# Kernel tuning notes

Hardware: AMD Instinct MI355X
Metric: run time of the kernel (lower is better)

The kernel has to match this reference:

```python
import jax, jax.numpy as jnp
import numpy as np

CANVAS = 512
SCORE_THR = 0.02
NMS_THR = 0.45
LVTOP = 1000      # cfg['lvtop'] for mm source
IMTOP = 200       # cfg['imtop']
NMS_PRE = 2000    # fixed pre-NMS candidate cap (static shape for jit)
NUM_CLASSES = 80
STRIDES = [8, 16, 32, 64, 128, 256, 512]
AR3 = [False, True, True, True, True, False, False]


def _make_priors():
    # get_scales(512): smallest=0.04, rmin=0.1, rmax=0.9, n=7
    smallest, rmin, rmax, n = 0.04, 0.1, 0.9, 7
    step = (rmax - rmin) / (n - 2)
    scales = [smallest] + [rmin + i * step for i in range(n)]
    sz = np.round(np.array(scales) * CANVAS).astype(np.int64)
    pr, lvlen = [], []
    for i, s in enumerate(STRIDES):
        fs = CANVAS // s
        ratios = [1.0, 2.0, 0.5] + ([3.0, 1.0 / 3.0] if AR3[i] else [])
        wh = [(sz[i] * np.sqrt(r), sz[i] / np.sqrt(r)) for r in ratios]
        extra = np.sqrt(float(sz[i]) * float(sz[i + 1]))  # sqrt(sz[i+1]/sz[i])*sz[i]
        wh.insert(1, (extra, extra))
        wh = np.array(wh, np.float32)            # [na, 2]
        xs = (np.arange(fs, dtype=np.float32) + 0.5) * s
        cx, cy = np.meshgrid(xs, xs)             # rows index y
        ctr = np.stack([cx, cy], -1)[:, :, None, :]  # [fs, fs, 1, 2]
        na = wh.shape[0]
        p = np.concatenate([np.broadcast_to(ctr, (fs, fs, na, 2)),
                            np.broadcast_to(wh, (fs, fs, na, 2))], -1).reshape(-1, 4)
        pr.append(p)
        lvlen.append(p.shape[0])
    return np.concatenate(pr).astype(np.float32), lvlen

PRIORS_NP, LVLEN = _make_priors()   # total 24564, lvlen=[16384,6144,1536,384,96,16,4]


def setup_inputs() -> dict:
    key = jax.random.key(0)
    k1, k2 = jax.random.split(key)
    A = PRIORS_NP.shape[0]
    cls_logits = jax.random.normal(k1, (4, A, NUM_CLASSES + 1), dtype=jnp.float32)
    reg = jax.random.normal(k2, (4, A, 4), dtype=jnp.float32)
    priors = jnp.asarray(PRIORS_NP)
    return {"cls_logits": cls_logits, "reg": reg, "priors": priors}


def _pairwise_iou(b):  # b: [K,4] xyxy
    area = (b[:, 2] - b[:, 0]) * (b[:, 3] - b[:, 1])
    lt = jnp.maximum(b[:, None, :2], b[None, :, :2])
    rb = jnp.minimum(b[:, None, 2:], b[None, :, 2:])
    wh = jnp.clip(rb - lt, 0.0)
    inter = wh[..., 0] * wh[..., 1]
    return inter / jnp.maximum(area[:, None] + area[None, :] - inter, 1e-6)


def _nms_keep(b):  # boxes sorted by descending score, class-offset applied
    m = _pairwise_iou(b) * jnp.triu(jnp.ones((NMS_PRE, NMS_PRE), b.dtype), 1)
    def body(sup, i):
        sup = sup | ((~sup[i]) & (m[i] > NMS_THR))
        return sup, None
    sup, _ = jax.lax.scan(body, jnp.zeros((NMS_PRE,), bool), jnp.arange(NMS_PRE))
    return ~sup


def reference(cls_logits, reg, priors):
    N = cls_logits.shape[0]
    C = NUM_CLASSES
    # softmax, background class is LAST (bckg_class_first=False for mm source)
    scr = jax.nn.softmax(cls_logits, axis=-1)[..., :-1]
    scr = jnp.where(scr > SCORE_THR, scr, 0.0)  # score threshold (fidx filter)
    # per-level top-k over flattened (anchor, class) pairs  [post.top_per_level]
    vals_l, anch_l, cls_l = [], [], []
    start = 0
    for lv in LVLEN:
        f = scr[:, start:start + lv, :].reshape(N, lv * C)
        k = min(LVTOP, lv * C)
        v, idx = jax.lax.top_k(f, k)
        vals_l.append(v)
        anch_l.append(start + idx // C)
        cls_l.append(idx % C)
        start += lv
    vals = jnp.concatenate(vals_l, 1)
    anch = jnp.concatenate(anch_l, 1)
    cls = jnp.concatenate(cls_l, 1)
    # fixed-size pre-NMS cap (static shapes under jit)
    v2, sel = jax.lax.top_k(vals, NMS_PRE)
    anch = jnp.take_along_axis(anch, sel, 1)
    cls = jnp.take_along_axis(cls, sel, 1)
    # decode boxes  [post.decode_boxes, mults=(0.1, 0.2), clamp=True]
    p = priors[anch]                                 # [N,K,4] cxcywh
    r = jnp.take_along_axis(reg, anch[..., None], 1)  # [N,K,4]
    cx = p[..., 0] + r[..., 0] * 0.1 * p[..., 2]
    cy = p[..., 1] + r[..., 1] * 0.1 * p[..., 3]
    w = p[..., 2] * jnp.exp(r[..., 2] * 0.2)
    h = p[..., 3] * jnp.exp(r[..., 3] * 0.2)
    boxes = jnp.stack([cx - w / 2, cy - h / 2, cx + w / 2, cy + h / 2], -1)
    boxes = jnp.clip(boxes, 0.0, float(CANVAS))
    # class-aware NMS via class offsets
    nb = boxes + cls.astype(boxes.dtype)[..., None] * (2.0 * CANVAS)
    keep = jax.vmap(_nms_keep)(nb)                   # [N,K] bool
    fs = jnp.where(keep & (v2 > 0), v2, 0.0)
    fv, fi = jax.lax.top_k(fs, IMTOP)                # imtop
    fb = jnp.take_along_axis(boxes, fi[..., None], 1)
    fc = jnp.take_along_axis(cls, fi, 1)
    fb = jnp.where(fv[..., None] > 0, fb, 0.0)
    return fb, fv, fc
```

## Files before the change

### kernel.cpp

```cpp
#include <hip/hip_runtime.h>
#include <hip/hip_bf16.h>
#include <math.h>

typedef unsigned long long u64;
typedef unsigned int u32;

#define A_TOTAL 24564
#define NCLS 80
#define NIMG 4
#define NPRE 2000
#define NLV 7
#define HBUCKETS 1024
#define BEXP_BASE 0x3CA3
#define TOTAL_G (NIMG * A_TOTAL)
#define FA 64
#define FT 256
#define NBLK_F ((TOTAL_G + FA - 1) / FA)
#define POOL_CAP_MAX 4096
#define CAPSEL 4608

__device__ __constant__ int c_klv[NLV] = {1000,1000,1000,1000,1000,1000,320};

#define WS_HIST      0
#define WS_MCOUNT    114688
#define WS_BCOUNT    114800
#define WS_ZERO_END  114912
#define WS_PCOUNT    114912
#define WS_MAIN      121280
#define WS_BND       350656
#define WS_BOXES     1268160
#define WS_CLS       1396160
#define WS_SCORE     1428160
#define WS_MASK      1460160
#define WS_POOL      3508160

#define NZERO_W (WS_ZERO_END / 4)

__device__ inline u64 shfl_u64(u64 v, int src) {
  int lo = __shfl((int)(u32)(v & 0xFFFFFFFFULL), src);
  int hi = __shfl((int)(u32)(v >> 32), src);
  return ((u64)(u32)hi << 32) | (u32)lo;
}

__device__ inline int score_bucket(u32 bits) {
  int b = (int)(bits >> 16) - BEXP_BASE;
  return b < 0 ? 0 : (b > HBUCKETS - 1 ? HBUCKETS - 1 : b);
}

__device__ inline int level_of(int a) {
  return (a < 16384) ? 0 : (a < 22528) ? 1 : (a < 24064) ? 2 :
         (a < 24448) ? 3 : (a < 24544) ? 4 : (a < 24560) ? 5 : 6;
}

__global__ __launch_bounds__(256) void k_zero(u32* __restrict__ p) {
  int i = blockIdx.x * 256 + threadIdx.x;
  if (i < NZERO_W) p[i] = 0;
}

__device__ inline void score20(const float* __restrict__ logits, int g, int q,
                               float (&e)[20], float& rt) {
  const float* row = logits + (size_t)g * 81;
  float x[20];
#pragma unroll
  for (int i = 0; i < 20; ++i) x[i] = row[q * 20 + i];
  float x80 = (q == 3) ? row[80] : 0.f;
  float mloc = x[0];
#pragma unroll
  for (int i = 1; i < 20; ++i) mloc = fmaxf(mloc, x[i]);
  if (q == 3) mloc = fmaxf(mloc, x80);
  float m = fmaxf(mloc, __shfl_xor(mloc, 1));
  m = fmaxf(m, __shfl_xor(m, 2));
  float tq = 0.f;
#pragma unroll
  for (int i = 0; i < 20; ++i) { e[i] = expf(x[i] - m); tq += e[i]; }
  if (q == 3) tq += expf(x80 - m);
  float t = tq + __shfl_xor(tq, 1);
  t = t + __shfl_xor(t, 2);
  rt = 1.0f / t;
}

__device__ inline void wave_find_cut(const u32* __restrict__ h, int k, int lane,
                                     int& cx, int& cy) {
  u32 s = 0;
#pragma unroll
  for (int i = 0; i < 16; ++i) s += h[lane * 16 + i];
  u32 S = s;
#pragma unroll
  for (int o = 1; o < 64; o <<= 1) {
    u32 t = (u32)__shfl_down((int)S, o);
    if (lane + o < 64) S += t;
  }
  u32 total = (u32)__shfl((int)S, 0);
  if (total <= (u32)k) { cx = -1; cy = 0; return; }
  u64 bm = __ballot(S >= (u32)k);
  int L0 = 63 - (int)__clzll((long long)bm);
  u32 Sup = (u32)__shfl_down((int)S, 1);
  if (lane == 63) Sup = 0;
  int rcx = 0, rcy = 0;
  if (lane == L0) {
    u32 cum = Sup;
    for (int i = 15; i >= 0; --i) {
      u32 c = h[lane * 16 + i];
      if (cum + c >= (u32)k) { rcx = lane * 16 + i; rcy = k - (int)cum; break; }
      cum += c;
    }
  }
  cx = __shfl(rcx, L0);
  cy = __shfl(rcy, L0);
}

__global__ __launch_bounds__(FT) void k_fused(const float* __restrict__ logits,
                                              u32* __restrict__ histG,
                                              u64* __restrict__ pool,
                                              u32* __restrict__ pcount, int cap) {
  __shared__ u32 sh[HBUCKETS];
  __shared__ int nm;
  int tid = threadIdx.x, bx = blockIdx.x;
  for (int b = tid; b < HBUCKETS; b += FT) sh[b] = 0;
  if (tid == 0) nm = 0;
  int la = tid >> 2, q = tid & 3;
  int g = bx * FA + la;
  bool valid = g < TOTAL_G;
  int g0 = bx * FA;
  int seg0 = (g0 / A_TOTAL) * NLV + level_of(g0 % A_TOTAL);
  int seg = seg0, a = 0;
  float e[20];
  float rt = 0.f;
  if (valid) {
    int img = g / A_TOTAL;
    a = g - img * A_TOTAL;
    seg = img * NLV + level_of(a);
    score20(logits, g, q, e, rt);
  }
  int uniform = __syncthreads_and((int)(!valid || seg == seg0));
  if (valid) {
    u32* hdst = uniform ? sh : (histG + (size_t)seg * HBUCKETS);
    int c0 = q * 20;
    u32 wmask = 0;
#pragma unroll
    for (int i = 0; i < 20; ++i) {
      float s = e[i] * rt;
      if (s > 0.02f) wmask |= (1u << i);
    }
    int cnt = __popc(wmask);
    int basep = 0;
    if (cnt) basep = atomicAdd(&nm, cnt);
    while (wmask) {
      int i = __ffs(wmask) - 1;
      wmask &= wmask - 1;
      float s = e[i] * rt;
      u32 bits = __float_as_uint(s);
      atomicAdd(&hdst[score_bucket(bits)], 1u);
      if (basep < cap)
        pool[(size_t)bx * cap + basep] =
            ((u64)bits << 32) | (u64)(0xFFFFFFFFu - (u32)(a * NCLS + c0 + i));
      ++basep;
    }
  }
  __syncthreads();
  if (uniform) {
    u32* hseg = histG + (size_t)seg0 * HBUCKETS;
    for (int b = tid; b < HBUCKETS; b += FT) {
      u32 v = sh[b];
      if (v) atomicAdd(&hseg[b], v);
    }
  }
  if (tid == 0) pcount[bx] = (u32)nm;
}

__global__ __launch_bounds__(FT) void k_filter(const float* __restrict__ logits,
                                               const u64* __restrict__ pool,
                                               const u32* __restrict__ pcount,
                                               const u32* __restrict__ histG, int cap,
                                               u64* __restrict__ mainG, u32* __restrict__ mcount,
                                               u64* __restrict__ bndG, u32* __restrict__ bcount) {
  __shared__ int lcx4[4];
  __shared__ u64 mk[1024]; __shared__ unsigned char msg_[1024];
  __shared__ u64 bkl[256]; __shared__ unsigned char bsg[256];
  __shared__ int nm, nb, cm[4], cb[4], basem[4], baseb[4], wm[4], wb[4];
  int tid = threadIdx.x, bx = blockIdx.x;
  if (tid < 4) { cm[tid] = 0; cb[tid] = 0; wm[tid] = 0; wb[tid] = 0; }
  if (tid == 0) { nm = 0; nb = 0; }
  int g0 = bx * FA;
  int img0 = g0 / A_TOTAL;
  int alo = g0 - img0 * A_TOTAL;
  int gN = g0 + FA - 1; if (gN > TOTAL_G - 1) gN = TOTAL_G - 1;
  int seg_lo = img0 * NLV + level_of(alo);
  int seg_hi = (gN / A_TOTAL) * NLV + level_of(gN % A_TOTAL);
  int nseg = seg_hi - seg_lo + 1;
  int wid = tid >> 6, lane = tid & 63;
  if (wid < nseg) {
    int cx, cy;
    wave_find_cut(histG + (size_t)(seg_lo + wid) * HBUCKETS,
                  c_klv[(seg_lo + wid) % NLV], lane, cx, cy);
    if (lane == 0) lcx4[wid] = cx;
  }
  __syncthreads();
  int n = (int)pcount[bx];
  if (n <= cap) {
    for (int t = tid; t < n; t += FT) {
      u64 key = pool[(size_t)bx * cap + t];
      u32 bits = (u32)(key >> 32);
      u32 flat = 0xFFFFFFFFu - (u32)(key & 0xFFFFFFFFULL);
      int a = (int)(flat / NCLS);
      int img = (a >= alo) ? img0 : img0 + 1;
      int seg = img * NLV + level_of(a);
      int si = seg - seg_lo;
      int ctx = lcx4[si];
      int bk = score_bucket(bits);
      if (ctx < 0 || bk > ctx) {
        int p = atomicAdd(&nm, 1);
        if (p < 1024) { mk[p] = key; msg_[p] = (unsigned char)si; atomicAdd(&cm[si], 1); }
        else { u32 pg = atomicAdd(&mcount[seg], 1u); if (pg < 1024) mainG[(size_t)seg * 1024 + pg] = key; }
      } else if (bk == ctx) {
        int p = atomicAdd(&nb, 1);
        if (p < 256) { bkl[p] = key; bsg[p] = (unsigned char)si; atomicAdd(&cb[si], 1); }
        else { u32 pg = atomicAdd(&bcount[seg], 1u); if (pg < 4096) bndG[(size_t)seg * 4096 + pg] = key; }
      }
    }
  } else {
    int la = tid >> 2, q = tid & 3;
    int g = g0 + la;
    if (g < TOTAL_G) {
      int img = g / A_TOTAL;
      int a = g - img * A_TOTAL;
      int seg = img * NLV + level_of(a);
      int si = seg - seg_lo;
      int ctx = lcx4[si];
      float e[20];
      float rt;
      score20(logits, g, q, e, rt);
      int c0 = q * 20;
      for (int i = 0; i < 20; ++i) {
        float s = e[i] * rt;
        if (s > 0.02f) {
          u32 bits = __float_as_uint(s);
          int bk = score_bucket(bits);
          u64 key = ((u64)bits << 32) | (u64)(0xFFFFFFFFu - (u32)(a * NCLS + c0 + i));
          if (ctx < 0 || bk > ctx) {
            int p = atomicAdd(&nm, 1);
            if (p < 1024) { mk[p] = key; msg_[p] = (unsigned char)si; atomicAdd(&cm[si], 1); }
            else { u32 pg = atomicAdd(&mcount[seg], 1u); if (pg < 1024) mainG[(size_t)seg * 1024 + pg] = key; }
          } else if (bk == ctx) {
            int p = atomicAdd(&nb, 1);
            if (p < 256) { bkl[p] = key; bsg[p] = (unsigned char)si; atomicAdd(&cb[si], 1); }
            else { u32 pg = atomicAdd(&bcount[seg], 1u); if (pg < 4096) bndG[(size_t)seg * 4096 + pg] = key; }
          }
        }
      }
    }
  }
  __syncthreads();
  if (tid < nseg) {
    if (cm[tid] > 0) basem[tid] = (int)atomicAdd(&mcount[seg_lo + tid], (u32)cm[tid]);
    if (cb[tid] > 0) baseb[tid] = (int)atomicAdd(&bcount[seg_lo + tid], (u32)cb[tid]);
  }
  __syncthreads();
  int tm = nm < 1024 ? nm : 1024;
  for (int idx = tid; idx < tm; idx += FT) {
    int si = msg_[idx];
    int slot = atomicAdd(&wm[si], 1);
    int d = basem[si] + slot;
    if (d < 1024) mainG[(size_t)(seg_lo + si) * 1024 + d] = mk[idx];
  }
  int tb = nb < 256 ? nb : 256;
  for (int idx = tid; idx < tb; idx += FT) {
    int si = bsg[idx];
    int slot = atomicAdd(&wb[si], 1);
    int d = baseb[si] + slot;
    if (d < 4096) bndG[(size_t)(seg_lo + si) * 4096 + d] = bkl[idx];
  }
}

__device__ inline void bitonic_desc(u64* s, int n) {
  for (int k = 2; k <= n; k <<= 1)
    for (int j = k >> 1; j > 0; j >>= 1) {
      __syncthreads();
      for (int i = threadIdx.x; i < n; i += blockDim.x) {
        int l = i ^ j;
        if (l > i) {
          u64 a = s[i], b = s[l];
          if (((i & k) == 0) ? (a < b) : (a > b)) { s[i] = b; s[l] = a; }
        }
      }
    }
  __syncthreads();
}

__global__ __launch_bounds__(1024) void k_refine(const u32* __restrict__ histG,
                                                 const u64* __restrict__ bndG,
                                                 const u32* __restrict__ bcount,
                                                 u64* __restrict__ mainG, u32* __restrict__ mcount) {
  int seg = blockIdx.x;
  __shared__ int sh_cx, sh_cy;
  __shared__ u64 s[4096];
  int tid = threadIdx.x, lane = tid & 63;
  if (tid < 64) {
    int cx, cy;
    wave_find_cut(histG + (size_t)seg * HBUCKETS, c_klv[seg % NLV], lane, cx, cy);
    if (lane == 0) { sh_cx = cx; sh_cy = cy; }
  }
  __syncthreads();
  if (sh_cx < 0) return;
  int m = (int)bcount[seg]; if (m > 4096) m = 4096;
  int n = 64; while (n < m) n <<= 1;
  for (int t = tid; t < n; t += 1024)
    s[t] = (t < m) ? bndG[(size_t)seg * 4096 + t] : 0ULL;
  bitonic_desc(s, n);
  int kp = sh_cy; if (kp > m) kp = m;
  int base = (int)mcount[seg];
  for (int t = tid; t < kp; t += 1024) {
    int p = base + t;
    if (p < 1024) mainG[(size_t)seg * 1024 + p] = s[t];
  }
  __syncthreads();
  if (tid == 0) {
    int nb = base + kp;
    mcount[seg] = (u32)(nb > 1024 ? 1024 : nb);
  }
}

__global__ __launch_bounds__(1024) void k_gsel(const u32* __restrict__ histG,
                                               const u64* __restrict__ mainG,
                                               const u32* __restrict__ mcount,
                                               const float4* __restrict__ priors,
                                               const float4* __restrict__ reg,
                                               float4* __restrict__ boxesG,
                                               int* __restrict__ clsG,
                                               float* __restrict__ scoreG) {
  int img = blockIdx.x;
  int tid = threadIdx.x, wid = tid >> 6, lane = tid & 63;
  __shared__ u32 H[HBUCKETS];
  __shared__ u32 cntb[HBUCKETS];
  __shared__ u32 Sarr[HBUCKETS];
  __shared__ u32 cnt2[HBUCKETS];
  __shared__ u64 sel[CAPSEL];
  __shared__ int lcx[NLV], lcy[NLV];
  __shared__ int sh_gx, sh_gy, sh_cC, sh_cand, sh_sgx;
  if (tid == 0) { sh_cC = 0; sh_cand = 0; sh_sgx = -1; }
  if (wid < NLV) {
    int cx, cy;
    wave_find_cut(histG + (size_t)(img * NLV + wid) * HBUCKETS, c_klv[wid], lane, cx, cy);
    if (lane == 0) { lcx[wid] = cx; lcy[wid] = cy; }
  }
  __syncthreads();
  for (int b = tid; b < HBUCKETS; b += 1024) {
    u32 acc = 0;
#pragma unroll
    for (int l = 0; l < NLV; ++l) {
      u32 h = histG[(size_t)(img * NLV + l) * HBUCKETS + b];
      int cx = lcx[l];
      if (cx < 0 || b > cx) acc += h;
      else if (b == cx) acc += (u32)lcy[l];
    }
    H[b] = acc;
    cntb[b] = 0;
    cnt2[b] = 0;
  }
  __syncthreads();
  if (wid == 0) {
    int gx, gy;
    wave_find_cut(H, NPRE, lane, gx, gy);
    if (lane == 0) { sh_gx = gx; sh_gy = gy; }
  }
  __syncthreads();
  int gx = sh_gx, gy = sh_gy;
  int mcap[NLV];
#pragma unroll
  for (int l = 0; l < NLV; ++l) { int c = (int)mcount[img * NLV + l]; mcap[l] = c > 1024 ? 1024 : c; }
  for (int l = 0; l < NLV; ++l)
    for (int t = tid; t < mcap[l]; t += 1024) {
      u64 key = mainG[(size_t)(img * NLV + l) * 1024 + t];
      int b = score_bucket((u32)(key >> 32));
      if (gx < 0 || b > gx) atomicAdd(&cntb[b], 1u);
      else if (b == gx) atomicAdd(&sh_cC, 1);
    }
  __syncthreads();
  for (int b = tid; b < HBUCKETS; b += 1024) Sarr[b] = cntb[b];
  __syncthreads();
  {
    u32* A = Sarr; u32* B = H;
    for (int o = 1; o < HBUCKETS; o <<= 1) {
      for (int b = tid; b < HBUCKETS; b += 1024)
        B[b] = A[b] + ((b + o < HBUCKETS) ? A[b + o] : 0u);
      __syncthreads();
      u32* tmp = A; A = B; B = tmp;
    }
  }
  int cA = (int)Sarr[0];
  int cC = sh_cC;
  int cand = (gx >= 0) ? cC : 0;
  int sgx = -1;
  if (gx >= 0 && cA + cC > CAPSEL) {
    for (int b = tid; b < HBUCKETS; b += 1024) H[b] = 0;
    __syncthreads();
    for (int l = 0; l < NLV; ++l)
      for (int t = tid; t < mcap[l]; t += 1024) {
        u64 key = mainG[(size_t)(img * NLV + l) * 1024 + t];
        u32 bits = (u32)(key >> 32);
        if (score_bucket(bits) == gx) atomicAdd(&H[(bits >> 6) & 1023], 1u);
      }
    __syncthreads();
    if (wid == 0) {
      int a1, a2;
      wave_find_cut(H, gy, lane, a1, a2);
      if (lane == 0) sh_sgx = a1;
    }
    __syncthreads();
    sgx = sh_sgx;
    if (sgx >= 0) {
      for (int s2 = tid; s2 < HBUCKETS; s2 += 1024)
        if (s2 >= sgx) { u32 v = H[s2]; if (v) atomicAdd(&sh_cand, (int)v); }
      __syncthreads();
      cand = sh_cand;
    }
    if (cA + cand > CAPSEL) cand = CAPSEL - cA;
  }
  __syncthreads();
  for (int l = 0; l < NLV; ++l)
    for (int t = tid; t < mcap[l]; t += 1024) {
      u64 key = mainG[(size_t)(img * NLV + l) * 1024 + t];
      u32 bits = (u32)(key >> 32);
      int b = score_bucket(bits);
      bool inc = false; int segbase = 0, seglen = 0;
      if (gx < 0 || b > gx) {
        inc = true; segbase = (int)(Sarr[b] - cntb[b]); seglen = (int)cntb[b];
      } else if (b == gx) {
        inc = (sgx < 0) || ((int)((bits >> 6) & 1023) >= sgx);
        segbase = (int)Sarr[b]; seglen = cand;
      }
      if (inc) {
        int slot = (int)atomicAdd(&cnt2[b], 1u);
        if (slot < seglen) sel[segbase + slot] = key;
      }
    }
  __syncthreads();
  int total = cA + cand;
  u64 myk[5]; int myp[5];
#pragma unroll
  for (int it = 0; it < 5; ++it) {
    int t = tid + it * 1024;
    myp[it] = -1; myk[it] = 0;
    if (t < total) {
      u64 key = sel[t];
      u32 bits = (u32)(key >> 32);
      int b = score_bucket(bits);
      int segbase, seglen;
      if (gx >= 0 && b == gx) { segbase = (int)Sarr[b]; seglen = cand; }
      else { segbase = (int)(Sarr[b] - cntb[b]); seglen = (int)cntb[b]; }
      int r = 0;
      for (int u = 0; u < seglen; ++u) r += (sel[segbase + u] > key) ? 1 : 0;
      myk[it] = key; myp[it] = segbase + r;
    }
  }
  __syncthreads();
#pragma unroll
  for (int it = 0; it < 5; ++it) if (myp[it] >= 0) sel[myp[it]] = myk[it];
  __syncthreads();
  for (int t = tid; t < NPRE; t += 1024) {
    u64 key = (t < total) ? sel[t] : 0ULL;
    float4 bx = make_float4(0.f, 0.f, 0.f, 0.f);
    int c = -1;
    float sc = 0.f;
    if (key != 0ULL) {
      sc = __uint_as_float((u32)(key >> 32));
      u32 flat = 0xFFFFFFFFu - (u32)(key & 0xFFFFFFFFULL);
      int a = (int)(flat / NCLS);
      c = (int)(flat % NCLS);
      float4 p = priors[a];
      float4 r = reg[(size_t)img * A_TOTAL + a];
      float cx = p.x + (r.x * 0.1f) * p.z;
      float cy = p.y + (r.y * 0.1f) * p.w;
      float w = p.z * expf(r.z * 0.2f);
      float h = p.w * expf(r.w * 0.2f);
      bx.x = fminf(fmaxf(cx - w * 0.5f, 0.f), 512.f);
      bx.y = fminf(fmaxf(cy - h * 0.5f, 0.f), 512.f);
      bx.z = fminf(fmaxf(cx + w * 0.5f, 0.f), 512.f);
      bx.w = fminf(fmaxf(cy + h * 0.5f, 0.f), 512.f);
    }
    boxesG[(size_t)img * NPRE + t] = bx;
    clsG[(size_t)img * NPRE + t] = c;
    scoreG[(size_t)img * NPRE + t] = sc;
  }
}

__global__ __launch_bounds__(256) void k_mask(const float4* __restrict__ boxesG,
                                              const int* __restrict__ clsG,
                                              u64* __restrict__ maskG) {
  __shared__ float4 lb[NPRE];
  __shared__ int lc[NPRE];
  int img = blockIdx.x / 500;
  int rb = (blockIdx.x % 500) * 4;
  for (int t = threadIdx.x; t < NPRE; t += 256) {
    lb[t] = boxesG[(size_t)img * NPRE + t];
    lc[t] = clsG[(size_t)img * NPRE + t];
  }
  __syncthreads();
  int w = threadIdx.x >> 6, lane = threadIdx.x & 63;
  int i = rb + w;
  float4 bi = lb[i];
  int ci = lc[i];
  float ai = (bi.z - bi.x) * (bi.w - bi.y);
  u64* mrow = maskG + ((size_t)img * NPRE + i) * 32;
  for (int ch = 0; ch < 32; ++ch) {
    int j = ch * 64 + lane;
    bool pred = false;
    if (j < NPRE && j > i) {
      if (lc[j] == ci) {
        float4 bj = lb[j];
        float xx1 = fmaxf(bi.x, bj.x), yy1 = fmaxf(bi.y, bj.y);
        float xx2 = fminf(bi.z, bj.z), yy2 = fminf(bi.w, bj.w);
        float ww = fmaxf(xx2 - xx1, 0.f), hh = fmaxf(yy2 - yy1, 0.f);
        float inter = ww * hh;
        float aj = (bj.z - bj.x) * (bj.w - bj.y);
        float iou = inter / fmaxf(ai + aj - inter, 1e-6f);
        pred = iou > 0.45f;
      }
    }
    u64 word = __ballot(pred);
    if (lane == 0) mrow[ch] = word;
  }
}

__global__ __launch_bounds__(256) void k_scanfinal(const u64* __restrict__ maskG,
                                                   const float4* __restrict__ boxesG,
                                                   const int* __restrict__ clsG,
                                                   const float* __restrict__ scoreG,
                                                   float* __restrict__ out) {
  int img = blockIdx.x;
  int tid = threadIdx.x;
  __shared__ u64 sh_remv[32];
  __shared__ u32 keptList[216];
  __shared__ int sh_cnt, sh_done;
  __shared__ int kpref[257];
  __shared__ unsigned short S[NPRE];
  if (tid == 0) { sh_cnt = 0; sh_done = 0; }
  __syncthreads();
  if (tid < 64) {
    int lane = tid;
    int wl = lane & 31;
    const u64* M = maskG + (size_t)img * NPRE * 32;
    u64 remv = 0;
    u64 cur[16], nxt[16];
    int cnt = 0;
#pragma unroll
    for (int r = 0; r < 16; ++r) cur[r] = M[(size_t)r * 32 + wl];
    int t = 0;
    for (; t < 125; ++t) {
      if (t < 124) {
#pragma unroll
        for (int r = 0; r < 16; ++r) nxt[r] = M[(size_t)((t + 1) * 16 + r) * 32 + wl];
      }
#pragma unroll
      for (int r = 0; r < 16; ++r) {
        int i = t * 16 + r;
        u64 rm = shfl_u64(remv, i >> 6);
        if (!((rm >> (i & 63)) & 1ULL)) {
          remv |= cur[r];
          if (lane == 0 && cnt < 216) keptList[cnt] = (u32)i;
          ++cnt;
        }
      }
#pragma unroll
      for (int r = 0; r < 16; ++r) cur[r] = nxt[r];
      if (cnt >= 200) { ++t; break; }
    }
    if (lane == 0) sh_cnt = cnt < 216 ? cnt : 216;
    if (t >= 125) {
      if (lane == 0) sh_done = 1;
      if (lane < 32) sh_remv[lane] = remv;
    }
  }
  __syncthreads();
  int nK = sh_cnt;
  if (sh_done && nK < 200) {
    int base = tid * 8;
    bool sb[8];
    int scnt = 0;
#pragma unroll
    for (int e = 0; e < 8; ++e) {
      int i = base + e;
      bool sup = (i < NPRE) && ((sh_remv[i >> 6] >> (i & 63)) & 1ULL);
      sb[e] = sup;
      scnt += sup ? 1 : 0;
    }
    kpref[tid + 1] = scnt;
    if (tid == 0) kpref[0] = 0;
    __syncthreads();
    if (tid == 0) {
      int acc = 0;
      for (int t = 1; t <= 256; ++t) { acc += kpref[t]; kpref[t] = acc; }
    }
    __syncthreads();
    int sp = kpref[tid];
#pragma unroll
    for (int e = 0; e < 8; ++e) {
      int i = base + e;
      if (i < NPRE && sb[e]) S[sp++] = (unsigned short)i;
    }
    __syncthreads();
    if (tid < 200) {
      float fv = 0.f;
      float4 fb = make_float4(0.f, 0.f, 0.f, 0.f);
      int fc;
      if (tid < nK) {
        int idx = (int)keptList[tid];
        fv = scoreG[(size_t)img * NPRE + idx];
        fb = boxesG[(size_t)img * NPRE + idx];
        fc = clsG[(size_t)img * NPRE + idx];
      } else {
        int idx = S[tid - nK];
        fc = clsG[(size_t)img * NPRE + idx];
      }
      float* fbo = out + (size_t)img * 800 + tid * 4;
      fbo[0] = fb.x; fbo[1] = fb.y; fbo[2] = fb.z; fbo[3] = fb.w;
      out[3200 + (size_t)img * 200 + tid] = fv;
      out[4000 + (size_t)img * 200 + tid] = (float)fc;
    }
  } else {
    if (tid < 200) {
      int idx = (int)keptList[tid];
      float fv = scoreG[(size_t)img * NPRE + idx];
      float4 fb = boxesG[(size_t)img * NPRE + idx];
      int fc = clsG[(size_t)img * NPRE + idx];
      float* fbo = out + (size_t)img * 800 + tid * 4;
      fbo[0] = fb.x; fbo[1] = fb.y; fbo[2] = fb.z; fbo[3] = fb.w;
      out[3200 + (size_t)img * 200 + tid] = fv;
      out[4000 + (size_t)img * 200 + tid] = (float)fc;
    }
  }
}

extern "C" void kernel_launch(void* const* d_in, const int* in_sizes, int n_in,
                              void* d_out, int out_size, void* d_ws, size_t ws_size,
                              hipStream_t stream) {
  const float* logits = (const float*)d_in[0];
  const float4* reg = (const float4*)d_in[1];
  const float4* priors = (const float4*)d_in[2];
  char* ws = (char*)d_ws;
  u32* hist = (u32*)(ws + WS_HIST);
  u32* mcount = (u32*)(ws + WS_MCOUNT);
  u32* bcount = (u32*)(ws + WS_BCOUNT);
  u32* pcount = (u32*)(ws + WS_PCOUNT);
  u64* mainL = (u64*)(ws + WS_MAIN);
  u64* bndL = (u64*)(ws + WS_BND);
  float4* boxes = (float4*)(ws + WS_BOXES);
  int* cls = (int*)(ws + WS_CLS);
  float* score = (float*)(ws + WS_SCORE);
  u64* mask = (u64*)(ws + WS_MASK);
  u64* pool = (u64*)(ws + WS_POOL);

  size_t avail = ws_size > (size_t)WS_POOL ? ws_size - (size_t)WS_POOL : 0;
  int cap = (int)(avail / ((size_t)NBLK_F * 8));
  if (cap > POOL_CAP_MAX) cap = POOL_CAP_MAX;

  k_zero<<<(NZERO_W + 255) / 256, 256, 0, stream>>>((u32*)d_ws);
  k_fused<<<NBLK_F, FT, 0, stream>>>(logits, hist, pool, pcount, cap);
  k_filter<<<NBLK_F, FT, 0, stream>>>(logits, pool, pcount, hist, cap,
                                      mainL, mcount, bndL, bcount);
  k_refine<<<28, 1024, 0, stream>>>(hist, bndL, bcount, mainL, mcount);
  k_gsel<<<NIMG, 1024, 0, stream>>>(hist, mainL, mcount, priors, reg, boxes, cls, score);
  k_mask<<<NIMG * 500, 256, 0, stream>>>(boxes, cls, mask);
  k_scanfinal<<<NIMG, 256, 0, stream>>>(mask, boxes, cls, score, (float*)d_out);
}
```

Measured before the change: 113.5 us.

## Fuse IoU mask computation and greedy NMS scan into one per-image kernel

Replaces the separate mask kernel (2000 blocks writing a full 2000x2000 bitmask to global memory) and the scan kernel with one 1024-thread block per image. Wave 0 runs the greedy suppression scan over 16-row chunks while the other 15 waves compute the next chunk's IoU mask rows into a double-buffered shared-memory buffer. Mask computation also stops early once 200 boxes are kept. This removes the global mask traffic and a kernel launch, but leaves only 4 blocks on the GPU and adds a block-wide barrier per chunk.

Measured after the change: 211.7 us. 86.4% more time.

```diff
diff --git a/kernel.cpp b/kernel.cpp
--- a/kernel.cpp
+++ b/kernel.cpp
@@ -18,6 +18,7 @@
 #define NBLK_F ((TOTAL_G + FA - 1) / FA)
 #define POOL_CAP_MAX 4096
 #define CAPSEL 4608
+#define NMST 1024
 
 __device__ __constant__ int c_klv[NLV] = {1000,1000,1000,1000,1000,1000,320};
 
@@ -31,7 +32,6 @@
 #define WS_BOXES     1268160
 #define WS_CLS       1396160
 #define WS_SCORE     1428160
-#define WS_MASK      1460160
 #define WS_POOL      3508160
 
 #define NZERO_W (WS_ZERO_END / 4)
@@ -484,29 +484,36 @@
   }
 }
 
-__global__ __launch_bounds__(256) void k_mask(const float4* __restrict__ boxesG,
+__global__ __launch_bounds__(NMST) void k_nms(const float4* __restrict__ boxesG,
                                               const int* __restrict__ clsG,
-                                              u64* __restrict__ maskG) {
+                                              const float* __restrict__ scoreG,
+                                              float* __restrict__ out) {
+  int img = blockIdx.x;
+  int tid = threadIdx.x, wid = tid >> 6, lane = tid & 63;
   __shared__ float4 lb[NPRE];
-  __shared__ int lc[NPRE];
-  int img = blockIdx.x / 500;
-  int rb = (blockIdx.x % 500) * 4;
-  for (int t = threadIdx.x; t < NPRE; t += 256) {
+  __shared__ short lc2[NPRE];
+  __shared__ u64 mbuf[2][16][32];
+  __shared__ u64 sh_remv[32];
+  __shared__ u32 keptList[216];
+  __shared__ int sh_cnt, sh_done, sh_stop;
+  __shared__ int kpref[NMST + 1];
+  __shared__ unsigned short S[NPRE];
+  if (tid == 0) { sh_cnt = 0; sh_done = 0; sh_stop = 0; }
+  for (int t = tid; t < NPRE; t += NMST) {
     lb[t] = boxesG[(size_t)img * NPRE + t];
-    lc[t] = clsG[(size_t)img * NPRE + t];
-  }
-  __syncthreads();
-  int w = threadIdx.x >> 6, lane = threadIdx.x & 63;
-  int i = rb + w;
-  float4 bi = lb[i];
-  int ci = lc[i];
-  float ai = (bi.z - bi.x) * (bi.w - bi.y);
-  u64* mrow = maskG + ((size_t)img * NPRE + i) * 32;
-  for (int ch = 0; ch < 32; ++ch) {
-    int j = ch * 64 + lane;
-    bool pred = false;
-    if (j < NPRE && j > i) {
-      if (lc[j] == ci) {
+    lc2[t] = (short)clsG[(size_t)img * NPRE + t];
+  }
+  __syncthreads();
+
+  auto row_mask = [&](int t, int buf, int r) {
+    int i = t * 16 + r;
+    float4 bi = lb[i];
+    short ci = lc2[i];
+    float ai = (bi.z - bi.x) * (bi.w - bi.y);
+    for (int c = 0; c < 32; ++c) {
+      int j = c * 64 + lane;
+      bool pred = false;
+      if (j > i && lc2[j] == ci) {
         float4 bj = lb[j];
         float xx1 = fmaxf(bi.x, bj.x), yy1 = fmaxf(bi.y, bj.y);
         float xx2 = fminf(bi.z, bj.z), yy2 = fminf(bi.w, bj.w);
@@ -516,88 +523,63 @@
         float iou = inter / fmaxf(ai + aj - inter, 1e-6f);
         pred = iou > 0.45f;
       }
-    }
-    u64 word = __ballot(pred);
-    if (lane == 0) mrow[ch] = word;
-  }
-}
-
-__global__ __launch_bounds__(256) void k_scanfinal(const u64* __restrict__ maskG,
-                                                   const float4* __restrict__ boxesG,
-                                                   const int* __restrict__ clsG,
-                                                   const float* __restrict__ scoreG,
-                                                   float* __restrict__ out) {
-  int img = blockIdx.x;
-  int tid = threadIdx.x;
-  __shared__ u64 sh_remv[32];
-  __shared__ u32 keptList[216];
-  __shared__ int sh_cnt, sh_done;
-  __shared__ int kpref[257];
-  __shared__ unsigned short S[NPRE];
-  if (tid == 0) { sh_cnt = 0; sh_done = 0; }
-  __syncthreads();
-  if (tid < 64) {
-    int lane = tid;
-    int wl = lane & 31;
-    const u64* M = maskG + (size_t)img * NPRE * 32;
-    u64 remv = 0;
-    u64 cur[16], nxt[16];
-    int cnt = 0;
-#pragma unroll
-    for (int r = 0; r < 16; ++r) cur[r] = M[(size_t)r * 32 + wl];
-    int t = 0;
-    for (; t < 125; ++t) {
-      if (t < 124) {
-#pragma unroll
-        for (int r = 0; r < 16; ++r) nxt[r] = M[(size_t)((t + 1) * 16 + r) * 32 + wl];
-      }
-#pragma unroll
+      u64 word = __ballot(pred);
+      if (lane == 0) mbuf[buf][r][c] = word;
+    }
+  };
+
+  row_mask(0, 0, wid);
+  __syncthreads();
+
+  u64 remv = 0;
+  int cnt = 0;
+  int t = 0;
+  while (true) {
+    if (wid > 0 && t + 1 < 125) {
+      for (int r = wid - 1; r < 16; r += 15) row_mask(t + 1, (t + 1) & 1, r);
+    }
+    if (wid == 0) {
+      int wl = lane & 31;
       for (int r = 0; r < 16; ++r) {
         int i = t * 16 + r;
+        u64 cur = mbuf[t & 1][r][wl];
         u64 rm = shfl_u64(remv, i >> 6);
         if (!((rm >> (i & 63)) & 1ULL)) {
-          remv |= cur[r];
+          remv |= cur;
           if (lane == 0 && cnt < 216) keptList[cnt] = (u32)i;
           ++cnt;
         }
       }
-#pragma unroll
-      for (int r = 0; r < 16; ++r) cur[r] = nxt[r];
-      if (cnt >= 200) { ++t; break; }
-    }
-    if (lane == 0) sh_cnt = cnt < 216 ? cnt : 216;
-    if (t >= 125) {
-      if (lane == 0) sh_done = 1;
-      if (lane < 32) sh_remv[lane] = remv;
-    }
-  }
-  __syncthreads();
+      if (lane == 0 && (cnt >= 200 || t == 124)) {
+        sh_stop = 1;
+        sh_cnt = cnt < 216 ? cnt : 216;
+        if (cnt < 200 && t == 124) sh_done = 1;
+      }
+      if (t == 124 && lane < 32) sh_remv[lane] = remv;
+    }
+    __syncthreads();
+    if (sh_stop) break;
+    ++t;
+  }
+
   int nK = sh_cnt;
   if (sh_done && nK < 200) {
-    int base = tid * 8;
-    bool sb[8];
+    int base = tid * 2;
+    bool sb0 = false, sb1 = false;
     int scnt = 0;
-#pragma unroll
-    for (int e = 0; e < 8; ++e) {
-      int i = base + e;
-      bool sup = (i < NPRE) && ((sh_remv[i >> 6] >> (i & 63)) & 1ULL);
-      sb[e] = sup;
-      scnt += sup ? 1 : 0;
-    }
+    if (base < NPRE)     { sb0 = (sh_remv[base >> 6] >> (base & 63)) & 1ULL; scnt += sb0 ? 1 : 0; }
+    if (base + 1 < NPRE) { sb1 = (sh_remv[(base + 1) >> 6] >> ((base + 1) & 63)) & 1ULL; scnt += sb1 ? 1 : 0; }
     kpref[tid + 1] = scnt;
     if (tid == 0) kpref[0] = 0;
     __syncthreads();
     if (tid == 0) {
       int acc = 0;
-      for (int t = 1; t <= 256; ++t) { acc += kpref[t]; kpref[t] = acc; }
+      for (int i = 1; i <= NMST; ++i) { acc += kpref[i]; kpref[i] = acc; }
     }
     __syncthreads();
     int sp = kpref[tid];
-#pragma unroll
-    for (int e = 0; e < 8; ++e) {
-      int i = base + e;
-      if (i < NPRE && sb[e]) S[sp++] = (unsigned short)i;
-    }
+    if (base < NPRE && sb0) S[sp++] = (unsigned short)base;
+    if (base + 1 < NPRE && sb1) S[sp++] = (unsigned short)(base + 1);
     __syncthreads();
     if (tid < 200) {
       float fv = 0.f;
@@ -606,11 +588,11 @@
       if (tid < nK) {
         int idx = (int)keptList[tid];
         fv = scoreG[(size_t)img * NPRE + idx];
-        fb = boxesG[(size_t)img * NPRE + idx];
-        fc = clsG[(size_t)img * NPRE + idx];
+        fb = lb[idx];
+        fc = (int)lc2[idx];
       } else {
         int idx = S[tid - nK];
-        fc = clsG[(size_t)img * NPRE + idx];
+        fc = (int)lc2[idx];
       }
       float* fbo = out + (size_t)img * 800 + tid * 4;
       fbo[0] = fb.x; fbo[1] = fb.y; fbo[2] = fb.z; fbo[3] = fb.w;
@@ -621,8 +603,8 @@
     if (tid < 200) {
       int idx = (int)keptList[tid];
       float fv = scoreG[(size_t)img * NPRE + idx];
-      float4 fb = boxesG[(size_t)img * NPRE + idx];
-      int fc = clsG[(size_t)img * NPRE + idx];
+      float4 fb = lb[idx];
+      int fc = (int)lc2[idx];
       float* fbo = out + (size_t)img * 800 + tid * 4;
       fbo[0] = fb.x; fbo[1] = fb.y; fbo[2] = fb.z; fbo[3] = fb.w;
       out[3200 + (size_t)img * 200 + tid] = fv;
@@ -647,7 +629,6 @@
   float4* boxes = (float4*)(ws + WS_BOXES);
   int* cls = (int*)(ws + WS_CLS);
   float* score = (float*)(ws + WS_SCORE);
-  u64* mask = (u64*)(ws + WS_MASK);
   u64* pool = (u64*)(ws + WS_POOL);
 
   size_t avail = ws_size > (size_t)WS_POOL ? ws_size - (size_t)WS_POOL : 0;
@@ -660,6 +641,5 @@
                                       mainL, mcount, bndL, bcount);
   k_refine<<<28, 1024, 0, stream>>>(hist, bndL, bcount, mainL, mcount);
   k_gsel<<<NIMG, 1024, 0, stream>>>(hist, mainL, mcount, priors, reg, boxes, cls, score);
-  k_mask<<<NIMG * 500, 256, 0, stream>>>(boxes, cls, mask);
-  k_scanfinal<<<NIMG, 256, 0, stream>>>(mask, boxes, cls, score, (float*)d_out);
-}
+  k_nms<<<NIMG, NMST, 0, stream>>>(boxes, cls, score, (float*)d_out);
+}
```

## Compute NMS mask only for first 512 rows with on-demand fallback

Applied to the files above, without the earlier changes.

The IoU suppression mask kernel now computes only the first 512 candidate rows per image instead of all 2000, which cuts its grid size roughly fourfold. The scan kernel walks these precomputed rows; if fewer than 200 boxes are kept by then, it computes the remaining rows tile by tile inside the scan block, reading boxes from global memory. Class ids are also stored as shorts in shared memory. The fallback path is slow and serialized but only runs when early termination fails.

Measured after the change: 107.3 us, median of 2. -5.5%, faster.

```diff
diff --git a/kernel.cpp b/kernel.cpp
--- a/kernel.cpp
+++ b/kernel.cpp
@@ -18,6 +18,8 @@
 #define NBLK_F ((TOTAL_G + FA - 1) / FA)
 #define POOL_CAP_MAX 4096
 #define CAPSEL 4608
+#define MROWS 512
+#define FTILES (MROWS / 16)
 
 __device__ __constant__ int c_klv[NLV] = {1000,1000,1000,1000,1000,1000,320};
 
@@ -488,20 +490,20 @@
                                               const int* __restrict__ clsG,
                                               u64* __restrict__ maskG) {
   __shared__ float4 lb[NPRE];
-  __shared__ int lc[NPRE];
-  int img = blockIdx.x / 500;
-  int rb = (blockIdx.x % 500) * 4;
+  __shared__ short lc[NPRE];
+  int img = blockIdx.x / (MROWS / 4);
+  int rb = (blockIdx.x % (MROWS / 4)) * 4;
   for (int t = threadIdx.x; t < NPRE; t += 256) {
     lb[t] = boxesG[(size_t)img * NPRE + t];
-    lc[t] = clsG[(size_t)img * NPRE + t];
+    lc[t] = (short)clsG[(size_t)img * NPRE + t];
   }
   __syncthreads();
   int w = threadIdx.x >> 6, lane = threadIdx.x & 63;
   int i = rb + w;
   float4 bi = lb[i];
-  int ci = lc[i];
+  short ci = lc[i];
   float ai = (bi.z - bi.x) * (bi.w - bi.y);
-  u64* mrow = maskG + ((size_t)img * NPRE + i) * 32;
+  u64* mrow = maskG + ((size_t)img * MROWS + i) * 32;
   for (int ch = 0; ch < 32; ++ch) {
     int j = ch * 64 + lane;
     bool pred = false;
@@ -529,25 +531,25 @@
                                                    float* __restrict__ out) {
   int img = blockIdx.x;
   int tid = threadIdx.x;
+  int wid = tid >> 6, lane = tid & 63;
   __shared__ u64 sh_remv[32];
+  __shared__ u64 fbm[16][32];
   __shared__ u32 keptList[216];
-  __shared__ int sh_cnt, sh_done;
+  __shared__ int sh_cnt, sh_done, sh_fall, sh_stop;
   __shared__ int kpref[257];
   __shared__ unsigned short S[NPRE];
-  if (tid == 0) { sh_cnt = 0; sh_done = 0; }
-  __syncthreads();
+  if (tid == 0) { sh_cnt = 0; sh_done = 0; sh_fall = 0; sh_stop = 0; }
+  __syncthreads();
+  u64 remv = 0;
+  int cnt = 0;
   if (tid < 64) {
-    int lane = tid;
     int wl = lane & 31;
-    const u64* M = maskG + (size_t)img * NPRE * 32;
-    u64 remv = 0;
+    const u64* M = maskG + (size_t)img * MROWS * 32;
     u64 cur[16], nxt[16];
-    int cnt = 0;
 #pragma unroll
     for (int r = 0; r < 16; ++r) cur[r] = M[(size_t)r * 32 + wl];
-    int t = 0;
-    for (; t < 125; ++t) {
-      if (t < 124) {
+    for (int t = 0; t < FTILES; ++t) {
+      if (t < FTILES - 1) {
 #pragma unroll
         for (int r = 0; r < 16; ++r) nxt[r] = M[(size_t)((t + 1) * 16 + r) * 32 + wl];
       }
@@ -563,12 +565,57 @@
       }
 #pragma unroll
       for (int r = 0; r < 16; ++r) cur[r] = nxt[r];
-      if (cnt >= 200) { ++t; break; }
-    }
-    if (lane == 0) sh_cnt = cnt < 216 ? cnt : 216;
-    if (t >= 125) {
-      if (lane == 0) sh_done = 1;
-      if (lane < 32) sh_remv[lane] = remv;
+      if (cnt >= 200) break;
+    }
+    if (lane == 0) { sh_cnt = cnt < 216 ? cnt : 216; sh_fall = (cnt < 200) ? 1 : 0; }
+  }
+  __syncthreads();
+  if (sh_fall) {
+    for (int ft = FTILES; ft < 125; ++ft) {
+      for (int r = wid; r < 16; r += 4) {
+        int i = ft * 16 + r;
+        float4 bi = boxesG[(size_t)img * NPRE + i];
+        int ci = clsG[(size_t)img * NPRE + i];
+        float ai = (bi.z - bi.x) * (bi.w - bi.y);
+        for (int ch = 0; ch < 32; ++ch) {
+          int j = ch * 64 + lane;
+          bool pred = false;
+          if (j < NPRE && j > i && clsG[(size_t)img * NPRE + j] == ci) {
+            float4 bj = boxesG[(size_t)img * NPRE + j];
+            float xx1 = fmaxf(bi.x, bj.x), yy1 = fmaxf(bi.y, bj.y);
+            float xx2 = fminf(bi.z, bj.z), yy2 = fminf(bi.w, bj.w);
+            float ww = fmaxf(xx2 - xx1, 0.f), hh = fmaxf(yy2 - yy1, 0.f);
+            float inter = ww * hh;
+            float aj = (bj.z - bj.x) * (bj.w - bj.y);
+            float iou = inter / fmaxf(ai + aj - inter, 1e-6f);
+            pred = iou > 0.45f;
+          }
+          u64 word = __ballot(pred);
+          if (lane == 0) fbm[r][ch] = word;
+        }
+      }
+      __syncthreads();
+      if (tid < 64) {
+        int wl = lane & 31;
+#pragma unroll
+        for (int r = 0; r < 16; ++r) {
+          int i = ft * 16 + r;
+          u64 rm = shfl_u64(remv, i >> 6);
+          if (!((rm >> (i & 63)) & 1ULL)) {
+            remv |= fbm[r][wl];
+            if (lane == 0 && cnt < 216) keptList[cnt] = (u32)i;
+            ++cnt;
+          }
+        }
+        if (lane == 0 && (cnt >= 200 || ft == 124)) {
+          sh_stop = 1;
+          sh_cnt = cnt < 216 ? cnt : 216;
+          if (cnt < 200) sh_done = 1;
+        }
+        if (ft == 124 && lane < 32) sh_remv[lane] = remv;
+      }
+      __syncthreads();
+      if (sh_stop) break;
     }
   }
   __syncthreads();
@@ -660,6 +707,6 @@
                                       mainL, mcount, bndL, bcount);
   k_refine<<<28, 1024, 0, stream>>>(hist, bndL, bcount, mainL, mcount);
   k_gsel<<<NIMG, 1024, 0, stream>>>(hist, mainL, mcount, priors, reg, boxes, cls, score);
-  k_mask<<<NIMG * 500, 256, 0, stream>>>(boxes, cls, mask);
+  k_mask<<<NIMG * (MROWS / 4), 256, 0, stream>>>(boxes, cls, mask);
   k_scanfinal<<<NIMG, 256, 0, stream>>>(mask, boxes, cls, score, (float*)d_out);
 }
```
